# Optimization experiments

Measured on AMD Instinct MI355X. Metric: run time of the kernel, lower is better.

The kernel has to match this reference:

```python
import jax, jax.numpy as jnp
import numpy as np

N = 50000          # nodes
E = 800000         # edges
H, C = 8, 32       # heads, channels per head
HC = H * C         # 256
IN = 4             # input feature dim
SLOPE = 0.2        # LeakyReLU negative slope (PyG default)
EPS = 1e-16        # PyG softmax denominator eps


def gat_layer(x, src, dst, ea, W, a_s, a_d, W_e, a_e, b, add_self_loops):
    """Single PyG-style GATConv with edge_dim=1. x:[N,in], ea:[E,1]."""
    if add_self_loops:
        # fill_value='mean': self-loop edge_attr = mean of incoming edge_attr per node
        ones = jnp.ones((src.shape[0], 1), ea.dtype)
        cnt = jax.ops.segment_sum(ones, dst, num_segments=N)
        loop_ea = jax.ops.segment_sum(ea, dst, num_segments=N) / jnp.maximum(cnt, 1.0)
        loop = jnp.arange(N, dtype=src.dtype)
        src = jnp.concatenate([src, loop])
        dst = jnp.concatenate([dst, loop])
        ea = jnp.concatenate([ea, loop_ea], axis=0)
    h = (x @ W).reshape(-1, H, C)                       # [N,H,C] shared src/dst proj
    al_s = jnp.einsum('nhc,hc->nh', h, a_s)              # [N,H]
    al_d = jnp.einsum('nhc,hc->nh', h, a_d)              # [N,H]
    # lin_edge is [1 -> H*C] with no bias, so (lin_edge(ea) * att_edge).sum(-1)
    # collapses to ea * w_e with w_e[h] = sum_c W_e[h,c]*a_e[h,c]
    w_e = jnp.sum(W_e * a_e, axis=-1)                    # [H]
    logits = al_s[src] + al_d[dst] + ea * w_e[None, :]   # [E,H]
    logits = jax.nn.leaky_relu(logits, SLOPE)
    # segment softmax over destination node
    m = jax.ops.segment_max(logits, dst, num_segments=N)
    m = jnp.where(jnp.isfinite(m), m, 0.0)
    p = jnp.exp(logits - m[dst])
    denom = jax.ops.segment_sum(p, dst, num_segments=N)
    alpha = p / (denom[dst] + EPS)                       # [E,H]
    out = jax.ops.segment_sum(h[src] * alpha[:, :, None], dst, num_segments=N)
    return out.reshape(-1, HC) + b                       # concat heads + bias


def setup_inputs() -> dict:
    key = jax.random.key(0)
    ks = jax.random.split(key, 24)
    inp = {
        'x': jax.random.normal(ks[0], (N, IN), jnp.float32),
        'edge_index': jax.random.randint(ks[1], (2, E), 0, N, jnp.int32),
        'edge_attr': jax.random.uniform(ks[2], (E, 1), jnp.float32),
    }
    in_dims = [IN, HC, HC]
    ki = 3
    for l in range(3):
        d = in_dims[l]
        inp[f'W{l+1}'] = jax.random.normal(ks[ki], (d, HC), jnp.float32) * (1.0 / np.sqrt(d)); ki += 1
        inp[f'as{l+1}'] = jax.random.normal(ks[ki], (H, C), jnp.float32) * 0.1; ki += 1
        inp[f'ad{l+1}'] = jax.random.normal(ks[ki], (H, C), jnp.float32) * 0.1; ki += 1
        inp[f'We{l+1}'] = jax.random.normal(ks[ki], (H, C), jnp.float32) * 0.1; ki += 1
        inp[f'ae{l+1}'] = jax.random.normal(ks[ki], (H, C), jnp.float32) * 0.1; ki += 1
        inp[f'b{l+1}'] = jnp.zeros((HC,), jnp.float32)
    return inp


def reference(x, edge_index, edge_attr,
              W1, as1, ad1, We1, ae1, b1,
              W2, as2, ad2, We2, ae2, b2,
              W3, as3, ad3, We3, ae3, b3):
    src, dst = edge_index[0], edge_index[1]
    h = jax.nn.relu(gat_layer(x, src, dst, edge_attr, W1, as1, ad1, We1, ae1, b1, False))
    h = jax.nn.relu(gat_layer(h, src, dst, edge_attr, W2, as2, ad2, We2, ae2, b2, True))
    h = jax.nn.relu(gat_layer(h, src, dst, edge_attr, W3, as3, ad3, We3, ae3, b3, True))
    return h
```

## Files before the change

kernel.cpp:

```cpp
#include <hip/hip_runtime.h>
#include <hip/hip_fp16.h>
#include <math.h>

#define HEADS 8
#define HC 256
#define SLOPE 0.2f
#define SM_EPS 1e-16f
#define LDA 40

typedef __attribute__((ext_vector_type(4))) _Float16 half4v;
typedef __attribute__((ext_vector_type(8))) _Float16 half8;
typedef __attribute__((ext_vector_type(4))) float f32x4;

__global__ void hist_kernel(const int* __restrict__ dst, int* __restrict__ cnt,
                            int* __restrict__ rank, int E) {
  int e = blockIdx.x * blockDim.x + threadIdx.x;
  if (e < E) rank[e] = atomicAdd(&cnt[dst[e]], 1);
}

__global__ void scan_blocks(const int* __restrict__ cnt, int* __restrict__ excl,
                            int* __restrict__ bsums, int N) {
  __shared__ int wsum[16];
  int t = threadIdx.x;
  int i = blockIdx.x * 1024 + t;
  int v = (i < N) ? cnt[i] : 0;
  int lane = t & 63, w = t >> 6;
  int s = v;
  #pragma unroll
  for (int off = 1; off < 64; off <<= 1) {
    int u = __shfl_up(s, off);
    if (lane >= off) s += u;
  }
  if (lane == 63) wsum[w] = s;
  __syncthreads();
  if (w == 0) {
    int ws = (lane < 16) ? wsum[lane] : 0;
    #pragma unroll
    for (int off = 1; off < 16; off <<= 1) {
      int u = __shfl_up(ws, off);
      if (lane >= off) ws += u;
    }
    if (lane < 16) wsum[lane] = ws;
  }
  __syncthreads();
  int wo = (w == 0) ? 0 : wsum[w - 1];
  int incl = s + wo;
  if (i < N) excl[i] = incl - v;
  if (t == 1023) bsums[blockIdx.x] = incl;
}

__global__ void scan_sums(int* __restrict__ bsums, int nb) {
  int lane = threadIdx.x;
  int carry = 0;
  for (int c0 = 0; c0 < nb; c0 += 64) {
    int idx = c0 + lane;
    int v = (idx < nb) ? bsums[idx] : 0;
    int s = v;
    #pragma unroll
    for (int off = 1; off < 64; off <<= 1) {
      int u = __shfl_up(s, off);
      if (lane >= off) s += u;
    }
    if (idx < nb) bsums[idx] = carry + s - v;
    carry += __shfl(s, 63);
  }
}

__global__ void scan_apply(const int* __restrict__ bsums, int* __restrict__ row_ptr,
                           int N, int E) {
  int i = blockIdx.x * blockDim.x + threadIdx.x;
  if (i < N) row_ptr[i] += bsums[i >> 10];
  if (i == 0) row_ptr[N] = E;
}

__global__ void fill_kernel(const int* __restrict__ src, const int* __restrict__ dst,
                            const float* __restrict__ ea, const int* __restrict__ row_ptr,
                            const int* __restrict__ rank, int2* __restrict__ srcea, int E) {
  int e = blockIdx.x * blockDim.x + threadIdx.x;
  if (e < E) {
    int pos = row_ptr[dst[e]] + rank[e];
    srcea[pos] = make_int2(src[e], __float_as_int(ea[e]));
  }
}

__global__ void wek_all(const float* __restrict__ We1, const float* __restrict__ ae1,
                        const float* __restrict__ We2, const float* __restrict__ ae2,
                        const float* __restrict__ We3, const float* __restrict__ ae3,
                        float* __restrict__ wev) {
  int l = blockIdx.x;
  int t = threadIdx.x;
  const float* We = (l == 0) ? We1 : (l == 1) ? We2 : We3;
  const float* ae = (l == 0) ? ae1 : (l == 1) ? ae2 : ae3;
  float p = 0.f;
  #pragma unroll
  for (int i = 0; i < 4; i++) p += We[t * 4 + i] * ae[t * 4 + i];
  p += __shfl_xor(p, 1);
  p += __shfl_xor(p, 2);
  p += __shfl_xor(p, 4);
  if ((t & 7) == 0) wev[l * 8 + (t >> 3)] = p;
}

__global__ void wsplit_kernel(const float* __restrict__ W, __half* __restrict__ WT) {
  int k = blockIdx.x;
  int n = threadIdx.x;
  WT[n * HC + k] = (__half)W[k * HC + n];
}

__global__ void gemm_fused(const float* __restrict__ A, const float* __restrict__ W,
                           const float* __restrict__ a_s, const float* __restrict__ a_d,
                           __half* __restrict__ Hh, float* __restrict__ als,
                           float* __restrict__ ald, int M, int K) {
  __shared__ float As[16][HC];
  int t = threadIdx.x;
  int m0 = blockIdx.x * 16;
  #pragma unroll
  for (int r = 0; r < 16; r++) {
    float v = 0.f;
    if (t < K && (m0 + r) < M) v = A[(size_t)(m0 + r) * K + t];
    As[r][t] = v;
  }
  __syncthreads();
  float acc[16];
  #pragma unroll
  for (int r = 0; r < 16; r++) acc[r] = 0.f;
  for (int k = 0; k < K; k += 4) {
    float w0 = W[(size_t)(k + 0) * HC + t];
    float w1 = W[(size_t)(k + 1) * HC + t];
    float w2 = W[(size_t)(k + 2) * HC + t];
    float w3 = W[(size_t)(k + 3) * HC + t];
    #pragma unroll
    for (int r = 0; r < 16; r++) {
      float4 a = *(const float4*)&As[r][k];
      acc[r] = fmaf(a.x, w0, acc[r]);
      acc[r] = fmaf(a.y, w1, acc[r]);
      acc[r] = fmaf(a.z, w2, acc[r]);
      acc[r] = fmaf(a.w, w3, acc[r]);
    }
  }
  float as_ = a_s[t], ad_ = a_d[t];
  #pragma unroll
  for (int r = 0; r < 16; r++) {
    int m = m0 + r;
    if (m < M) {
      Hh[(size_t)m * HC + t] = (__half)acc[r];
      float ps = acc[r] * as_;
      float pd = acc[r] * ad_;
      #pragma unroll
      for (int mm = 1; mm < 32; mm <<= 1) {
        ps += __shfl_xor(ps, mm);
        pd += __shfl_xor(pd, mm);
      }
      if ((t & 31) == 0) {
        als[(size_t)m * HEADS + (t >> 5)] = ps;
        ald[(size_t)m * HEADS + (t >> 5)] = pd;
      }
    }
  }
}

__global__ __launch_bounds__(256) void mfma_gemm(
    const __half* __restrict__ A, const __half* __restrict__ WT,
    const float* __restrict__ a_s, const float* __restrict__ a_d,
    __half* __restrict__ Hh, float* __restrict__ als, float* __restrict__ ald, int M) {
  __shared__ _Float16 sA[64 * LDA], sB[128 * LDA];
  int t = threadIdx.x;
  int bm = blockIdx.x >> 1, bn = blockIdx.x & 1;
  int m0 = bm * 64, n0 = bn * 128;
  int wave = t >> 6, lane = t & 63, quad = lane >> 4, l16 = lane & 15;
  int sr = t >> 2;
  int sk = (t & 3) * 8;

  f32x4 acc[8];
  #pragma unroll
  for (int c = 0; c < 8; c++) acc[c] = (f32x4){0.f, 0.f, 0.f, 0.f};

  size_t ar = (size_t)min(m0 + sr, M - 1) * HC;
  size_t br0 = (size_t)(n0 + sr) * HC;
  size_t br1 = (size_t)(n0 + sr + 64) * HC;

  half8 pA = *(const half8*)(A + ar + sk);
  half8 pB0 = *(const half8*)(WT + br0 + sk);
  half8 pB1 = *(const half8*)(WT + br1 + sk);

  for (int k0 = 0; k0 < HC; k0 += 32) {
    __syncthreads();
    *(half8*)(sA + sr * LDA + sk) = pA;
    *(half8*)(sB + sr * LDA + sk) = pB0;
    *(half8*)(sB + (sr + 64) * LDA + sk) = pB1;
    __syncthreads();
    int kn = k0 + 32;
    if (kn < HC) {
      pA = *(const half8*)(A + ar + kn + sk);
      pB0 = *(const half8*)(WT + br0 + kn + sk);
      pB1 = *(const half8*)(WT + br1 + kn + sk);
    }
    half8 av = *(const half8*)(sA + (wave * 16 + l16) * LDA + quad * 8);
    #pragma unroll
    for (int c = 0; c < 8; c++) {
      half8 bv = *(const half8*)(sB + (c * 16 + l16) * LDA + quad * 8);
      acc[c] = __builtin_amdgcn_mfma_f32_16x16x32_f16(av, bv, acc[c], 0, 0, 0);
    }
  }

  float asv[8], adv[8];
  #pragma unroll
  for (int c = 0; c < 8; c++) {
    int col = n0 + c * 16 + l16;
    asv[c] = a_s[col];
    adv[c] = a_d[col];
  }
  #pragma unroll
  for (int reg = 0; reg < 4; reg++) {
    int m = m0 + wave * 16 + quad * 4 + reg;
    bool ok = (m < M);
    if (ok) {
      #pragma unroll
      for (int c = 0; c < 8; c++)
        Hh[(size_t)m * HC + n0 + c * 16 + l16] = (__half)acc[c][reg];
    }
    #pragma unroll
    for (int d = 0; d < 4; d++) {
      float ps = acc[2 * d][reg] * asv[2 * d] + acc[2 * d + 1][reg] * asv[2 * d + 1];
      float pd = acc[2 * d][reg] * adv[2 * d] + acc[2 * d + 1][reg] * adv[2 * d + 1];
      #pragma unroll
      for (int mm = 1; mm < 16; mm <<= 1) {
        ps += __shfl_xor(ps, mm);
        pd += __shfl_xor(pd, mm);
      }
      if (ok && l16 == 0) {
        als[(size_t)m * HEADS + (n0 >> 5) + d] = ps;
        ald[(size_t)m * HEADS + (n0 >> 5) + d] = pd;
      }
    }
  }
}

template <int SELF, int SPLIT>
__global__ __launch_bounds__(256) void accum_kernel(
    const int2* __restrict__ srcea, const int* __restrict__ row_ptr,
    const __half* __restrict__ h, const float* __restrict__ als,
    const float* __restrict__ ald, const float* __restrict__ wev,
    const float* __restrict__ bias, float* __restrict__ out,
    __half* __restrict__ Ah, int N) {
  int n = blockIdx.x * 4 + (threadIdx.x >> 6);
  if (n >= N) return;
  int lane = threadIdx.x & 63;
  int h_t = lane >> 3;
  int base = row_ptr[n], deg = row_ptr[n + 1] - base;
  int ubase = __builtin_amdgcn_readfirstlane(base);
  int udeg = __builtin_amdgcn_readfirstlane(deg);
  float ald_h = ald[(size_t)n * HEADS + h_t];
  float we_h = wev[h_t];

  float den = 0.f, easum = 0.f;
  float4 acc = make_float4(0.f, 0.f, 0.f, 0.f);
  #pragma unroll 8
  for (int j = 0; j < udeg; j++) {
    int2 se = srcea[ubase + j];
    int s = se.x;
    float eav = __int_as_float(se.y);
    if (SELF) easum += eav;
    float l = als[(size_t)s * HEADS + h_t] + ald_h + eav * we_h;
    l = (l > 0.f) ? l : SLOPE * l;
    float p = __expf(l);
    den += p;
    const half4v hv = *(const half4v*)(h + (size_t)s * HC + lane * 4);
    acc.x = fmaf(p, (float)hv.x, acc.x);
    acc.y = fmaf(p, (float)hv.y, acc.y);
    acc.z = fmaf(p, (float)hv.z, acc.z);
    acc.w = fmaf(p, (float)hv.w, acc.w);
  }
  if (SELF) {
    float mean_ea = easum / fmaxf((float)udeg, 1.0f);
    float l = als[(size_t)n * HEADS + h_t] + ald_h + mean_ea * we_h;
    l = (l > 0.f) ? l : SLOPE * l;
    float p = __expf(l);
    den += p;
    const half4v hv = *(const half4v*)(h + (size_t)n * HC + lane * 4);
    acc.x = fmaf(p, (float)hv.x, acc.x);
    acc.y = fmaf(p, (float)hv.y, acc.y);
    acc.z = fmaf(p, (float)hv.z, acc.z);
    acc.w = fmaf(p, (float)hv.w, acc.w);
  }

  float rinv = 1.0f / (den + SM_EPS);
  int cbase = lane * 4;
  float4 o;
  o.x = fmaxf(fmaf(acc.x, rinv, bias[cbase + 0]), 0.f);
  o.y = fmaxf(fmaf(acc.y, rinv, bias[cbase + 1]), 0.f);
  o.z = fmaxf(fmaf(acc.z, rinv, bias[cbase + 2]), 0.f);
  o.w = fmaxf(fmaf(acc.w, rinv, bias[cbase + 3]), 0.f);
  if (SPLIT) {
    half4v hv;
    hv.x = (_Float16)o.x;
    hv.y = (_Float16)o.y;
    hv.z = (_Float16)o.z;
    hv.w = (_Float16)o.w;
    *(half4v*)(Ah + (size_t)n * HC + cbase) = hv;
  } else {
    *(float4*)(out + (size_t)n * HC + cbase) = o;
  }
}

extern "C" void kernel_launch(void* const* d_in, const int* in_sizes, int n_in,
                              void* d_out, int out_size, void* d_ws, size_t ws_size,
                              hipStream_t stream) {
  const float* x = (const float*)d_in[0];
  const int* ei = (const int*)d_in[1];
  const float* ea = (const float*)d_in[2];
  int N = in_sizes[0] / 4;
  int E = in_sizes[1] / 2;
  const int* src = ei;
  const int* dst = ei + E;

  const float* W[3];
  const float* Asw[3];
  const float* Adw[3];
  const float* Wew[3];
  const float* Aew[3];
  const float* Bw[3];
  for (int l = 0; l < 3; l++) {
    W[l]   = (const float*)d_in[3 + 6 * l + 0];
    Asw[l] = (const float*)d_in[3 + 6 * l + 1];
    Adw[l] = (const float*)d_in[3 + 6 * l + 2];
    Wew[l] = (const float*)d_in[3 + 6 * l + 3];
    Aew[l] = (const float*)d_in[3 + 6 * l + 4];
    Bw[l]  = (const float*)d_in[3 + 6 * l + 5];
  }

  char* w = (char*)d_ws;
  auto alloc = [&](size_t bytes) {
    char* p = w;
    w += (bytes + 255) & ~(size_t)255;
    return p;
  };
  __half* Hh    = (__half*)alloc((size_t)N * HC * 2);
  __half* Ah    = (__half*)alloc((size_t)N * HC * 2);
  int2* srcea   = (int2*)alloc((size_t)E * 8);
  int* rank     = (int*)alloc((size_t)E * 4);
  __half* WT2   = (__half*)alloc((size_t)HC * HC * 2);
  __half* WT3   = (__half*)alloc((size_t)HC * HC * 2);
  float* als    = (float*)alloc((size_t)N * HEADS * 4);
  float* ald    = (float*)alloc((size_t)N * HEADS * 4);
  float* wev    = (float*)alloc(24 * 4);
  int* cnt      = (int*)alloc((size_t)N * 4);
  int* row_ptr  = (int*)alloc(((size_t)N + 1) * 4);
  int* bsums    = (int*)alloc(((size_t)N / 1024 + 2) * 4);
  float* outf = (float*)d_out;

  int nb = (N + 1023) / 1024;
  (void)hipMemsetAsync(cnt, 0, (size_t)N * 4, stream);
  hist_kernel<<<(E + 255) / 256, 256, 0, stream>>>(dst, cnt, rank, E);
  scan_blocks<<<nb, 1024, 0, stream>>>(cnt, row_ptr, bsums, N);
  scan_sums<<<1, 64, 0, stream>>>(bsums, nb);
  scan_apply<<<(N + 255) / 256, 256, 0, stream>>>(bsums, row_ptr, N, E);
  fill_kernel<<<(E + 255) / 256, 256, 0, stream>>>(src, dst, ea, row_ptr, rank,
                                                   srcea, E);
  wek_all<<<3, 64, 0, stream>>>(Wew[0], Aew[0], Wew[1], Aew[1], Wew[2], Aew[2], wev);
  wsplit_kernel<<<HC, HC, 0, stream>>>(W[1], WT2);
  wsplit_kernel<<<HC, HC, 0, stream>>>(W[2], WT3);

  int agg_grid = (N + 3) / 4;
  int gemm_grid = ((N + 63) / 64) * 2;

  gemm_fused<<<(N + 15) / 16, 256, 0, stream>>>(x, W[0], Asw[0], Adw[0], Hh, als, ald, N, 4);
  accum_kernel<0, 1><<<agg_grid, 256, 0, stream>>>(srcea, row_ptr, Hh, als, ald,
                                                   wev + 0, Bw[0], nullptr, Ah, N);

  mfma_gemm<<<gemm_grid, 256, 0, stream>>>(Ah, WT2, Asw[1], Adw[1], Hh, als, ald, N);
  accum_kernel<1, 1><<<agg_grid, 256, 0, stream>>>(srcea, row_ptr, Hh, als, ald,
                                                   wev + 8, Bw[1], nullptr, Ah, N);

  mfma_gemm<<<gemm_grid, 256, 0, stream>>>(Ah, WT3, Asw[2], Adw[2], Hh, als, ald, N);
  accum_kernel<1, 0><<<agg_grid, 256, 0, stream>>>(srcea, row_ptr, Hh, als, ald,
                                                   wev + 16, Bw[2], outf, nullptr, N);
}
```

Before: 466.0 us.

## Recompute layer-1 features from 4-dim input inside aggregation instead of gathering fp16 H

Layer 1 no longer writes the N x 256 fp16 projection. The prep kernel computes only the attention logits, and the aggregation kernel gathers the 16-byte x row per neighbor and recomputes the projection with the 4x256 weight held in registers. This replaces a 512-byte gather per edge with a 16-byte gather plus a few FMAs, and also removes the H write. The remaining accumulate kernel loses its SELF template flag, since the self-loop path now always runs for layers 2 and 3.

```diff
diff --git a/kernel.cpp b/kernel.cpp
--- a/kernel.cpp
+++ b/kernel.cpp
@@ -106,45 +106,24 @@
   WT[n * HC + k] = (__half)W[k * HC + n];
 }
 
-__global__ void gemm_fused(const float* __restrict__ A, const float* __restrict__ W,
-                           const float* __restrict__ a_s, const float* __restrict__ a_d,
-                           __half* __restrict__ Hh, float* __restrict__ als,
-                           float* __restrict__ ald, int M, int K) {
-  __shared__ float As[16][HC];
+__global__ void l1_prep(const float* __restrict__ x, const float* __restrict__ W,
+                        const float* __restrict__ a_s, const float* __restrict__ a_d,
+                        float* __restrict__ als, float* __restrict__ ald, int M) {
+  __shared__ float4 Xs[16];
   int t = threadIdx.x;
   int m0 = blockIdx.x * 16;
-  #pragma unroll
-  for (int r = 0; r < 16; r++) {
-    float v = 0.f;
-    if (t < K && (m0 + r) < M) v = A[(size_t)(m0 + r) * K + t];
-    As[r][t] = v;
-  }
+  if (t < 16 && (m0 + t) < M) Xs[t] = *(const float4*)(x + (size_t)(m0 + t) * 4);
   __syncthreads();
-  float acc[16];
-  #pragma unroll
-  for (int r = 0; r < 16; r++) acc[r] = 0.f;
-  for (int k = 0; k < K; k += 4) {
-    float w0 = W[(size_t)(k + 0) * HC + t];
-    float w1 = W[(size_t)(k + 1) * HC + t];
-    float w2 = W[(size_t)(k + 2) * HC + t];
-    float w3 = W[(size_t)(k + 3) * HC + t];
-    #pragma unroll
-    for (int r = 0; r < 16; r++) {
-      float4 a = *(const float4*)&As[r][k];
-      acc[r] = fmaf(a.x, w0, acc[r]);
-      acc[r] = fmaf(a.y, w1, acc[r]);
-      acc[r] = fmaf(a.z, w2, acc[r]);
-      acc[r] = fmaf(a.w, w3, acc[r]);
-    }
-  }
+  float w0 = W[0 * HC + t], w1 = W[1 * HC + t], w2 = W[2 * HC + t], w3 = W[3 * HC + t];
   float as_ = a_s[t], ad_ = a_d[t];
   #pragma unroll
   for (int r = 0; r < 16; r++) {
     int m = m0 + r;
     if (m < M) {
-      Hh[(size_t)m * HC + t] = (__half)acc[r];
-      float ps = acc[r] * as_;
-      float pd = acc[r] * ad_;
+      float4 a = Xs[r];
+      float h = a.x * w0 + a.y * w1 + a.z * w2 + a.w * w3;
+      float ps = h * as_;
+      float pd = h * ad_;
       #pragma unroll
       for (int mm = 1; mm < 32; mm <<= 1) {
         ps += __shfl_xor(ps, mm);
@@ -235,7 +214,64 @@
   }
 }
 
-template <int SELF, int SPLIT>
+__global__ __launch_bounds__(256) void accum_l1_kernel(
+    const int2* __restrict__ srcea, const int* __restrict__ row_ptr,
+    const float* __restrict__ x, const float* __restrict__ W,
+    const float* __restrict__ als, const float* __restrict__ ald,
+    const float* __restrict__ wev, const float* __restrict__ bias,
+    __half* __restrict__ Ah, int N) {
+  int n = blockIdx.x * 4 + (threadIdx.x >> 6);
+  if (n >= N) return;
+  int lane = threadIdx.x & 63;
+  int h_t = lane >> 3;
+  int cbase = lane * 4;
+  int base = row_ptr[n], deg = row_ptr[n + 1] - base;
+  int ubase = __builtin_amdgcn_readfirstlane(base);
+  int udeg = __builtin_amdgcn_readfirstlane(deg);
+  float ald_h = ald[(size_t)n * HEADS + h_t];
+  float we_h = wev[h_t];
+  float4 wr0 = *(const float4*)(W + 0 * HC + cbase);
+  float4 wr1 = *(const float4*)(W + 1 * HC + cbase);
+  float4 wr2 = *(const float4*)(W + 2 * HC + cbase);
+  float4 wr3 = *(const float4*)(W + 3 * HC + cbase);
+
+  float den = 0.f;
+  float4 acc = make_float4(0.f, 0.f, 0.f, 0.f);
+  #pragma unroll 8
+  for (int j = 0; j < udeg; j++) {
+    int2 se = srcea[ubase + j];
+    int s = __builtin_amdgcn_readfirstlane(se.x);
+    float eav = __int_as_float(se.y);
+    float l = als[(size_t)s * HEADS + h_t] + ald_h + eav * we_h;
+    l = (l > 0.f) ? l : SLOPE * l;
+    float p = __expf(l);
+    den += p;
+    float4 xv = *(const float4*)(x + (size_t)s * 4);
+    float h0 = xv.x * wr0.x + xv.y * wr1.x + xv.z * wr2.x + xv.w * wr3.x;
+    float h1 = xv.x * wr0.y + xv.y * wr1.y + xv.z * wr2.y + xv.w * wr3.y;
+    float h2 = xv.x * wr0.z + xv.y * wr1.z + xv.z * wr2.z + xv.w * wr3.z;
+    float h3 = xv.x * wr0.w + xv.y * wr1.w + xv.z * wr2.w + xv.w * wr3.w;
+    acc.x = fmaf(p, h0, acc.x);
+    acc.y = fmaf(p, h1, acc.y);
+    acc.z = fmaf(p, h2, acc.z);
+    acc.w = fmaf(p, h3, acc.w);
+  }
+
+  float rinv = 1.0f / (den + SM_EPS);
+  float4 o;
+  o.x = fmaxf(fmaf(acc.x, rinv, bias[cbase + 0]), 0.f);
+  o.y = fmaxf(fmaf(acc.y, rinv, bias[cbase + 1]), 0.f);
+  o.z = fmaxf(fmaf(acc.z, rinv, bias[cbase + 2]), 0.f);
+  o.w = fmaxf(fmaf(acc.w, rinv, bias[cbase + 3]), 0.f);
+  half4v hv;
+  hv.x = (_Float16)o.x;
+  hv.y = (_Float16)o.y;
+  hv.z = (_Float16)o.z;
+  hv.w = (_Float16)o.w;
+  *(half4v*)(Ah + (size_t)n * HC + cbase) = hv;
+}
+
+template <int SPLIT>
 __global__ __launch_bounds__(256) void accum_kernel(
     const int2* __restrict__ srcea, const int* __restrict__ row_ptr,
     const __half* __restrict__ h, const float* __restrict__ als,
@@ -259,7 +295,7 @@
     int2 se = srcea[ubase + j];
     int s = se.x;
     float eav = __int_as_float(se.y);
-    if (SELF) easum += eav;
+    easum += eav;
     float l = als[(size_t)s * HEADS + h_t] + ald_h + eav * we_h;
     l = (l > 0.f) ? l : SLOPE * l;
     float p = __expf(l);
@@ -270,7 +306,7 @@
     acc.z = fmaf(p, (float)hv.z, acc.z);
     acc.w = fmaf(p, (float)hv.w, acc.w);
   }
-  if (SELF) {
+  {
     float mean_ea = easum / fmaxf((float)udeg, 1.0f);
     float l = als[(size_t)n * HEADS + h_t] + ald_h + mean_ea * we_h;
     l = (l > 0.f) ? l : SLOPE * l;
@@ -363,15 +399,15 @@
   int agg_grid = (N + 3) / 4;
   int gemm_grid = ((N + 63) / 64) * 2;
 
-  gemm_fused<<<(N + 15) / 16, 256, 0, stream>>>(x, W[0], Asw[0], Adw[0], Hh, als, ald, N, 4);
-  accum_kernel<0, 1><<<agg_grid, 256, 0, stream>>>(srcea, row_ptr, Hh, als, ald,
-                                                   wev + 0, Bw[0], nullptr, Ah, N);
+  l1_prep<<<(N + 15) / 16, 256, 0, stream>>>(x, W[0], Asw[0], Adw[0], als, ald, N);
+  accum_l1_kernel<<<agg_grid, 256, 0, stream>>>(srcea, row_ptr, x, W[0], als, ald,
+                                                wev + 0, Bw[0], Ah, N);
 
   mfma_gemm<<<gemm_grid, 256, 0, stream>>>(Ah, WT2, Asw[1], Adw[1], Hh, als, ald, N);
-  accum_kernel<1, 1><<<agg_grid, 256, 0, stream>>>(srcea, row_ptr, Hh, als, ald,
-                                                   wev + 8, Bw[1], nullptr, Ah, N);
+  accum_kernel<1><<<agg_grid, 256, 0, stream>>>(srcea, row_ptr, Hh, als, ald,
+                                                wev + 8, Bw[1], nullptr, Ah, N);
 
   mfma_gemm<<<gemm_grid, 256, 0, stream>>>(Ah, WT3, Asw[2], Adw[2], Hh, als, ald, N);
-  accum_kernel<1, 0><<<agg_grid, 256, 0, stream>>>(srcea, row_ptr, Hh, als, ald,
-                                                   wev + 16, Bw[2], outf, nullptr, N);
-}
+  accum_kernel<0><<<agg_grid, 256, 0, stream>>>(srcea, row_ptr, Hh, als, ald,
+                                                wev + 16, Bw[2], outf, nullptr, N);
+}
```

After: 446.3 us. -4.2%, faster.
